# Performance work log

Measured on AMD Instinct MI355X. Metric: run time of the kernel, lower is better.

The kernel has to match this reference:

```python
import jax, jax.numpy as jnp
import numpy as np

B, S, F = 4, 2048, 512
H, DH, OUT = 8, 64, 512  # attention_dim=512 -> head_dim=64
NEG_SLOPE = 0.01


def setup_inputs() -> dict:
    key = jax.random.key(0)
    ks = jax.random.split(key, 9)
    sc_in = 1.0 / np.sqrt(F)
    sc_hd = 1.0 / np.sqrt(H * DH)
    return {
        "x": jax.random.normal(ks[0], (B, S, F), dtype=jnp.float32),
        "Wq": jax.random.normal(ks[1], (F, H, DH), dtype=jnp.float32) * sc_in,
        "bq": jnp.zeros((H, DH), dtype=jnp.float32),
        "Wk": jax.random.normal(ks[2], (F, H, DH), dtype=jnp.float32) * sc_in,
        "bk": jnp.zeros((H, DH), dtype=jnp.float32),
        "Wv": jax.random.normal(ks[3], (F, H, DH), dtype=jnp.float32) * sc_in,
        "bv": jnp.zeros((H, DH), dtype=jnp.float32),
        "Wo": jax.random.normal(ks[4], (H, DH, OUT), dtype=jnp.float32) * sc_hd,
        "bo": jnp.zeros((OUT,), dtype=jnp.float32),
    }


def reference(x, Wq, bq, Wk, bk, Wv, bv, Wo, bo):
    # QKV projections: DenseGeneral(axis=-1, features=(H, DH)) -> [B, S, H, DH]
    q = jnp.einsum('bsf,fhd->bshd', x, Wq) + bq
    k = jnp.einsum('bsf,fhd->bshd', x, Wk) + bk
    v = jnp.einsum('bsf,fhd->bshd', x, Wv) + bv

    # Pairwise squared L2: l2[b,h,i,j] = ||q[b,i,h]-k[b,j,h]||^2
    q2 = jnp.sum(q * q, axis=-1)              # [B, S, H]
    k2 = jnp.sum(k * k, axis=-1)              # [B, S, H]
    qk = jnp.einsum('bihd,bjhd->bhij', q, k)  # [B, H, S, S]
    l2 = (q2.transpose(0, 2, 1)[:, :, :, None]
          + k2.transpose(0, 2, 1)[:, :, None, :]
          - 2.0 * qk)

    # softmax over key axis j, then weights.T @ value (note the transpose:
    # output token index is j, summed over query index i, as in the original)
    w = jax.nn.softmax(-l2, axis=-1)                  # [B, H, Si, Sj]
    attn = jnp.einsum('bhij,bihd->bjhd', w, v)        # [B, S, H, DH]

    # out DenseGeneral contracting (H, DH)
    out = jnp.einsum('bshd,hdo->bso', attn, Wo) + bo
    return jnp.where(out >= 0, out, NEG_SLOPE * out)
```

## Files before the change

### kernel.cpp

```cpp
#include <hip/hip_runtime.h>


typedef __attribute__((ext_vector_type(8))) short bf16x8;
typedef __attribute__((ext_vector_type(4))) float f32x4;
typedef __attribute__((ext_vector_type(4))) unsigned short u16x4;

#define MFMA16 __builtin_amdgcn_mfma_f32_16x16x32_bf16
#define LOG2E 1.4426950408889634f
#define TWO_LOG2E 2.8853900817779268f

__device__ inline unsigned short f2bf(float f) {
  unsigned int u = __float_as_uint(f);
  unsigned int r = 0x7fffu + ((u >> 16) & 1u);
  return (unsigned short)((u + r) >> 16);
}
__device__ inline float bf2f(unsigned short h) {
  return __uint_as_float(((unsigned int)h) << 16);
}
__device__ inline float fexp2(float x) { return __builtin_amdgcn_exp2f(x); }

__device__ inline void gl_lds16(const unsigned short* g, unsigned short* lds) {
  __builtin_amdgcn_global_load_lds(
      (const __attribute__((address_space(1))) unsigned int*)g,
      (__attribute__((address_space(3))) unsigned int*)lds, 16, 0, 0);
}

#define NXB4 (8192*512/4)

__global__ __launch_bounds__(256) void prep(
    const float* __restrict__ x, const float* __restrict__ bq,
    const float* __restrict__ bk, const float* __restrict__ bv,
    unsigned short* __restrict__ xb, float* __restrict__ biasp) {
  int i = blockIdx.x * blockDim.x + threadIdx.x;
  if (i < NXB4) {
    f32x4 v = ((const f32x4*)x)[i];
    u16x4 o;
    o.x = f2bf(v.x); o.y = f2bf(v.y); o.z = f2bf(v.z); o.w = f2bf(v.w);
    ((u16x4*)xb)[i] = o;
    return;
  }
  i -= NXB4;
  if (i < 1536) {
    biasp[i] = (i < 512) ? bq[i] : (i < 1024) ? bk[i - 512] : bv[i - 1024];
  }
}

__global__ __launch_bounds__(256) void packW(
    const float* __restrict__ Wq, const float* __restrict__ Wk,
    const float* __restrict__ Wv, const float* __restrict__ Wo,
    unsigned short* __restrict__ wqkvT, unsigned short* __restrict__ woT) {
  const int m = blockIdx.x >> 6;
  const int n0 = ((blockIdx.x >> 3) & 7) * 64;
  const int f0 = (blockIdx.x & 7) * 64;
  const float* W = (m == 0) ? Wq : (m == 1) ? Wk : (m == 2) ? Wv : Wo;
  __shared__ float tile[64][65];
  const int t = threadIdx.x;
  const int c = t & 63, r4 = t >> 6;
#pragma unroll
  for (int k = 0; k < 16; ++k) {
    const int r = r4 + k * 4;
    tile[r][c] = W[(size_t)(f0 + r) * 512 + n0 + c];
  }
  __syncthreads();
#pragma unroll
  for (int k = 0; k < 16; ++k) {
    const int n_idx = r4 + k * 4, f_idx = c;
    const unsigned short v = f2bf(tile[f_idx][n_idx]);
    if (m < 3)
      wqkvT[(size_t)(m * 512 + n0 + n_idx) * 512 + f0 + f_idx] = v;
    else
      woT[(size_t)(n0 + n_idx) * 512 + f0 + f_idx] = v;
  }
}

template<int MODE>
__global__ __launch_bounds__(256) void gemm_bt(
    const unsigned short* __restrict__ A, const unsigned short* __restrict__ Bt,
    const float* __restrict__ bias,
    unsigned short* __restrict__ o_q, unsigned short* __restrict__ o_k,
    unsigned short* __restrict__ o_v, float* __restrict__ o_f, int K) {
  const int lid = blockIdx.x + blockIdx.y * gridDim.x;
  const int tot = gridDim.x * gridDim.y;
  const int lid2 = (lid & 7) * (tot >> 3) + (lid >> 3);
  const int m0 = (lid2 / gridDim.x) * 128;
  const int n0 = (lid2 % gridDim.x) * 128;
  const int tid = threadIdx.x;
  const int w = tid >> 6, l = tid & 63, lg = l >> 4, ll = l & 15;
  const int wr = w >> 1, wc = w & 1;
  __shared__ unsigned short a_lds[128 * 32];
  __shared__ unsigned short b_lds[128 * 32];
  f32x4 acc[4][4] = {};
  const int nkt = K >> 5;
  for (int kt = 0; kt < nkt; ++kt) {
#pragma unroll
    for (int c = 0; c < 2; ++c) {
      const int cc_base = c * 256 + w * 64;
      const int cc = cc_base + l;
      const int row = cc >> 2, cl = cc & 3;
      gl_lds16(A + (size_t)(m0 + row) * K + kt * 32 + cl * 8, a_lds + cc_base * 8);
      gl_lds16(Bt + (size_t)(n0 + row) * K + kt * 32 + cl * 8, b_lds + cc_base * 8);
    }
    __syncthreads();
    bf16x8 af[4], bfr[4];
#pragma unroll
    for (int mi = 0; mi < 4; ++mi)
      af[mi] = *(const bf16x8*)(a_lds + (wr * 64 + mi * 16 + ll) * 32 + lg * 8);
#pragma unroll
    for (int ni = 0; ni < 4; ++ni)
      bfr[ni] = *(const bf16x8*)(b_lds + (wc * 64 + ni * 16 + ll) * 32 + lg * 8);
#pragma unroll
    for (int mi = 0; mi < 4; ++mi)
#pragma unroll
      for (int ni = 0; ni < 4; ++ni)
        acc[mi][ni] = MFMA16(af[mi], bfr[ni], acc[mi][ni], 0, 0, 0);
    __syncthreads();
  }
#pragma unroll
  for (int mi = 0; mi < 4; ++mi)
#pragma unroll
    for (int ni = 0; ni < 4; ++ni) {
      const int col = n0 + wc * 64 + ni * 16 + ll;
      const float bb = bias[col];
#pragma unroll
      for (int r = 0; r < 4; ++r) {
        const int row = m0 + wr * 64 + mi * 16 + lg * 4 + r;
        float v = acc[mi][ni][r] + bb;
        if (MODE == 0) {
          const int which = col >> 9, h = (col >> 6) & 7, d = col & 63;
          const int b = row >> 11, s = row & 2047;
          if (which == 0) v *= TWO_LOG2E;
          const size_t idx = ((size_t)((b * 8 + h) * 2048 + s)) * 64 + d;
          (which == 0 ? o_q : which == 1 ? o_k : o_v)[idx] = f2bf(v);
        } else {
          v = v >= 0.f ? v : 0.01f * v;
          o_f[(size_t)row * 512 + col] = v;
        }
      }
    }
}

__global__ __launch_bounds__(256) void k2_kernel(const unsigned short* __restrict__ k_g,
                                                 float* __restrict__ k2l_g) {
  const int lane = threadIdx.x & 63;
  const int wid = (blockIdx.x * blockDim.x + threadIdx.x) >> 6;
  const int nw = (gridDim.x * blockDim.x) >> 6;
  for (int row = wid; row < 32 * 2048; row += nw) {
    float v = bf2f(k_g[(size_t)row * 64 + lane]);
    v *= v;
#pragma unroll
    for (int m = 1; m < 64; m <<= 1) v += __shfl_xor(v, m);
    if (lane == 0) k2l_g[row] = LOG2E * v;
  }
}

__global__ __launch_bounds__(256) void transpose_v(const unsigned short* __restrict__ v_g,
                                                   const float* __restrict__ invl_g,
                                                   unsigned short* __restrict__ vt_g) {
  const int bh = blockIdx.x >> 5, st = blockIdx.x & 31;
  const int s0 = st * 64;
  __shared__ unsigned short tile[64][72];
  const int t = threadIdx.x;
  {
    const int sl = t >> 2, cg = t & 3;
    const float sc = invl_g[bh * 2048 + s0 + sl];
    const unsigned short* src = v_g + ((size_t)(bh * 2048 + s0 + sl)) * 64 + cg * 16;
    bf16x8 v0 = *(const bf16x8*)(src);
    bf16x8 v1 = *(const bf16x8*)(src + 8);
#pragma unroll
    for (int e = 0; e < 8; ++e) tile[sl][cg * 16 + e] = f2bf(sc * bf2f((unsigned short)v0[e]));
#pragma unroll
    for (int e = 0; e < 8; ++e) tile[sl][cg * 16 + 8 + e] = f2bf(sc * bf2f((unsigned short)v1[e]));
  }
  __syncthreads();
  {
    const int dl = t >> 2, sg = t & 3;
    bf16x8 o0, o1;
#pragma unroll
    for (int e = 0; e < 8; ++e) o0[e] = (short)tile[sg * 16 + e][dl];
#pragma unroll
    for (int e = 0; e < 8; ++e) o1[e] = (short)tile[sg * 16 + 8 + e][dl];
    unsigned short* dst = vt_g + ((size_t)(bh * 64 + dl)) * 2048 + s0 + sg * 16;
    *(bf16x8*)dst = o0;
    *(bf16x8*)(dst + 8) = o1;
  }
}

__global__ __launch_bounds__(256) void pass1(const unsigned short* __restrict__ q_g,
                                             const unsigned short* __restrict__ k_g,
                                             const float* __restrict__ k2l_g,
                                             float* __restrict__ invl_g) {
  const int bx = blockIdx.x;
  const int bh = (bx & 7) * 4 + ((bx >> 3) >> 4);
  const int ib = (bx >> 3) & 15;
  const int i0 = ib * 128;
  const int tid = threadIdx.x, w = tid >> 6, l = tid & 63, lg = l >> 4, ll = l & 15;
  __shared__ unsigned short k_lds[2][64 * 64];
  __shared__ float k2_lds[2][64];
  const unsigned short* k_bh = k_g + (size_t)bh * 2048 * 64;
  const unsigned short* qrow = q_g + ((size_t)(bh * 2048 + i0 + w * 32 + ll)) * 64;
  const bf16x8 qa00 = *(const bf16x8*)(qrow + lg * 8);
  const bf16x8 qa01 = *(const bf16x8*)(qrow + 32 + lg * 8);
  const bf16x8 qa10 = *(const bf16x8*)(qrow + 1024 + lg * 8);
  const bf16x8 qa11 = *(const bf16x8*)(qrow + 1024 + 32 + lg * 8);
  float lrun0[4] = {0.f, 0.f, 0.f, 0.f};
  float lrun1[4] = {0.f, 0.f, 0.f, 0.f};
  const int cb0 = w * 64, cb1 = 256 + w * 64;
  const int cc0 = cb0 + l, cc1 = cb1 + l;
  const int r0_ = cc0 >> 3, c0_ = cc0 & 7, r1_ = cc1 >> 3, c1_ = cc1 & 7;
  const int so0 = (c0_ ^ (r0_ & 7)) * 8;
  const int so1 = (c1_ ^ (r1_ & 7)) * 8;
  gl_lds16(k_bh + (size_t)r0_ * 64 + so0, &k_lds[0][cb0 * 8]);
  gl_lds16(k_bh + (size_t)r1_ * 64 + so1, &k_lds[0][cb1 * 8]);
  if (tid < 64) k2_lds[0][tid] = k2l_g[bh * 2048 + tid];
  __syncthreads();
  for (int jt = 0; jt < 32; ++jt) {
    const int slot = jt & 1;
    if (jt + 1 < 32) {
      const int j1 = (jt + 1) * 64;
      gl_lds16(k_bh + (size_t)(j1 + r0_) * 64 + so0, &k_lds[slot ^ 1][cb0 * 8]);
      gl_lds16(k_bh + (size_t)(j1 + r1_) * 64 + so1, &k_lds[slot ^ 1][cb1 * 8]);
      if (tid < 64) k2_lds[slot ^ 1][tid] = k2l_g[bh * 2048 + j1 + tid];
    }
#pragma unroll
    for (int nf = 0; nf < 4; ++nf) {
      const int jr = nf * 16 + ll;
      const unsigned short* kb = &k_lds[slot][jr * 64];
      const int sw = jr & 7;
      bf16x8 b0 = *(const bf16x8*)(kb + ((lg ^ sw) * 8));
      bf16x8 b1 = *(const bf16x8*)(kb + (((4 + lg) ^ sw) * 8));
      f32x4 sa0 = {};
      sa0 = MFMA16(qa00, b0, sa0, 0, 0, 0);
      sa0 = MFMA16(qa01, b1, sa0, 0, 0, 0);
      f32x4 sa1 = {};
      sa1 = MFMA16(qa10, b0, sa1, 0, 0, 0);
      sa1 = MFMA16(qa11, b1, sa1, 0, 0, 0);
      const float k2v = k2_lds[slot][jr];
      lrun0[0] += fexp2(sa0[0] - k2v);
      lrun0[1] += fexp2(sa0[1] - k2v);
      lrun0[2] += fexp2(sa0[2] - k2v);
      lrun0[3] += fexp2(sa0[3] - k2v);
      lrun1[0] += fexp2(sa1[0] - k2v);
      lrun1[1] += fexp2(sa1[1] - k2v);
      lrun1[2] += fexp2(sa1[2] - k2v);
      lrun1[3] += fexp2(sa1[3] - k2v);
    }
    __syncthreads();
  }
#pragma unroll
  for (int r = 0; r < 4; ++r) {
    float t0 = lrun0[r], t1 = lrun1[r];
#pragma unroll
    for (int m = 1; m < 16; m <<= 1) { t0 += __shfl_xor(t0, m); t1 += __shfl_xor(t1, m); }
    if (ll == 0) {
      invl_g[bh * 2048 + i0 + w * 32 + lg * 4 + r] = 1.f / t0;
      invl_g[bh * 2048 + i0 + w * 32 + 16 + lg * 4 + r] = 1.f / t1;
    }
  }
}

__global__ __launch_bounds__(256) void pass2(const unsigned short* __restrict__ q_g,
                                             const unsigned short* __restrict__ k_g,
                                             const unsigned short* __restrict__ vt_g,
                                             const float* __restrict__ k2l_g,
                                             unsigned short* __restrict__ part0,
                                             unsigned short* __restrict__ part1,
                                             unsigned short* __restrict__ part2) {
  const int bx = blockIdx.x;
  const int bh = (bx & 7) * 4 + ((bx >> 3) >> 4);
  const int jb = (bx >> 3) & 15;
  const int by = blockIdx.y;
  const int j0 = jb * 128;
  const int it0 = by * 11;
  const int it_end = (by == 2) ? 32 : it0 + 11;
  const int tid = threadIdx.x, w = tid >> 6, l = tid & 63, lg = l >> 4, ll = l & 15;
  __shared__ unsigned short q_lds[2][64 * 64];
  __shared__ unsigned short vt_lds[2][64 * 64];
  __shared__ unsigned short p_lds[128 * 64];
  const unsigned short* q_base = q_g + (size_t)bh * 2048 * 64;
  const unsigned short* vt_base = vt_g + (size_t)bh * 64 * 2048;
  const unsigned short* krow = k_g + ((size_t)(bh * 2048 + j0 + w * 32 + ll)) * 64;
  const bf16x8 ka00 = *(const bf16x8*)(krow + lg * 8);
  const bf16x8 ka01 = *(const bf16x8*)(krow + 32 + lg * 8);
  const bf16x8 ka10 = *(const bf16x8*)(krow + 1024 + lg * 8);
  const bf16x8 ka11 = *(const bf16x8*)(krow + 1024 + 32 + lg * 8);
  float k2v0[4], k2v1[4];
#pragma unroll
  for (int r = 0; r < 4; ++r) {
    k2v0[r] = k2l_g[bh * 2048 + j0 + w * 32 + lg * 4 + r];
    k2v1[r] = k2l_g[bh * 2048 + j0 + w * 32 + 16 + lg * 4 + r];
  }
  f32x4 oacc0[4] = {};
  f32x4 oacc1[4] = {};
  const int pslot = it0 & 1;
#pragma unroll
  for (int c = 0; c < 2; ++c) {
    const int cc_base = c * 256 + w * 64;
    const int cc = cc_base + l;
    const int row = cc >> 3, cl = cc & 7;
    const int csw = (cl ^ (row & 7)) * 8;
    gl_lds16(q_base + (size_t)(it0 * 64 + row) * 64 + csw, &q_lds[pslot][cc_base * 8]);
    gl_lds16(vt_base + (size_t)row * 2048 + it0 * 64 + csw, &vt_lds[pslot][cc_base * 8]);
  }
  __syncthreads();
  for (int it = it0; it < it_end; ++it) {
    const int slot = it & 1;
    if (it + 1 < it_end) {
      const int i1 = (it + 1) * 64;
#pragma unroll
      for (int c = 0; c < 2; ++c) {
        const int cc_base = c * 256 + w * 64;
        const int cc = cc_base + l;
        const int row = cc >> 3, cl = cc & 7;
        const int csw = (cl ^ (row & 7)) * 8;
        gl_lds16(q_base + (size_t)(i1 + row) * 64 + csw, &q_lds[slot ^ 1][cc_base * 8]);
        gl_lds16(vt_base + (size_t)row * 2048 + i1 + csw, &vt_lds[slot ^ 1][cc_base * 8]);
      }
    }
#pragma unroll
    for (int nf = 0; nf < 4; ++nf) {
      const int ir = nf * 16 + ll;
      const unsigned short* qb = &q_lds[slot][ir * 64];
      const int sw = ir & 7;
      bf16x8 b0 = *(const bf16x8*)(qb + ((lg ^ sw) * 8));
      bf16x8 b1 = *(const bf16x8*)(qb + (((4 + lg) ^ sw) * 8));
      f32x4 sa0 = {};
      sa0 = MFMA16(ka00, b0, sa0, 0, 0, 0);
      sa0 = MFMA16(ka01, b1, sa0, 0, 0, 0);
      f32x4 sa1 = {};
      sa1 = MFMA16(ka10, b0, sa1, 0, 0, 0);
      sa1 = MFMA16(ka11, b1, sa1, 0, 0, 0);
#pragma unroll
      for (int r = 0; r < 4; ++r) {
        const float p0 = fexp2(sa0[r] - k2v0[r]);
        const float p1 = fexp2(sa1[r] - k2v1[r]);
        const int ja = w * 32 + lg * 4 + r;
        const int jb2 = ja + 16;
        p_lds[ja * 64 + (ir ^ ((ja & 7) << 3))] =
            (unsigned short)(__float_as_uint(p0) >> 16);
        p_lds[jb2 * 64 + (ir ^ ((jb2 & 7) << 3))] =
            (unsigned short)(__float_as_uint(p1) >> 16);
      }
    }
    {
      const int jr0 = w * 32 + ll;
      const int jr1 = jr0 + 16;
      const int swp = ll & 7;
      const unsigned short* pb0 = p_lds + jr0 * 64;
      const unsigned short* pb1 = p_lds + jr1 * 64;
      bf16x8 pa00 = *(const bf16x8*)(pb0 + ((lg ^ swp) * 8));
      bf16x8 pa01 = *(const bf16x8*)(pb0 + (((4 + lg) ^ swp) * 8));
      bf16x8 pa10 = *(const bf16x8*)(pb1 + ((lg ^ swp) * 8));
      bf16x8 pa11 = *(const bf16x8*)(pb1 + (((4 + lg) ^ swp) * 8));
#pragma unroll
      for (int nf = 0; nf < 4; ++nf) {
        const int dr = nf * 16 + ll;
        const unsigned short* vb = &vt_lds[slot][dr * 64];
        const int sw = dr & 7;
        bf16x8 v0 = *(const bf16x8*)(vb + ((lg ^ sw) * 8));
        bf16x8 v1 = *(const bf16x8*)(vb + (((4 + lg) ^ sw) * 8));
        oacc0[nf] = MFMA16(pa00, v0, oacc0[nf], 0, 0, 0);
        oacc0[nf] = MFMA16(pa01, v1, oacc0[nf], 0, 0, 0);
        oacc1[nf] = MFMA16(pa10, v0, oacc1[nf], 0, 0, 0);
        oacc1[nf] = MFMA16(pa11, v1, oacc1[nf], 0, 0, 0);
      }
    }
    __syncthreads();
  }
  unsigned short* po = (by == 0) ? part0 : (by == 1) ? part1 : part2;
  const int b = bh >> 3, h2 = bh & 7;
#pragma unroll
  for (int nf = 0; nf < 4; ++nf) {
    const int d = nf * 16 + ll;
#pragma unroll
    for (int r = 0; r < 4; ++r) {
      const int j = j0 + w * 32 + lg * 4 + r;
      po[((size_t)(b * 2048 + j)) * 512 + h2 * 64 + d] = f2bf(oacc0[nf][r]);
      po[((size_t)(b * 2048 + j + 16)) * 512 + h2 * 64 + d] = f2bf(oacc1[nf][r]);
    }
  }
}

__global__ __launch_bounds__(256) void combine3(unsigned short* __restrict__ p0,
                                                const unsigned short* __restrict__ p1,
                                                const unsigned short* __restrict__ p2) {
  const int i = blockIdx.x * blockDim.x + threadIdx.x;
  bf16x8 a = ((const bf16x8*)p0)[i];
  bf16x8 b = ((const bf16x8*)p1)[i];
  bf16x8 c = ((const bf16x8*)p2)[i];
  bf16x8 o;
#pragma unroll
  for (int e = 0; e < 8; ++e)
    o[e] = (short)f2bf(bf2f((unsigned short)a[e]) + bf2f((unsigned short)b[e]) +
                       bf2f((unsigned short)c[e]));
  ((bf16x8*)p0)[i] = o;
}

extern "C" void kernel_launch(void* const* d_in, const int* in_sizes, int n_in,
                              void* d_out, int out_size, void* d_ws, size_t ws_size,
                              hipStream_t stream) {
  const float* x  = (const float*)d_in[0];
  const float* Wq = (const float*)d_in[1];
  const float* bq = (const float*)d_in[2];
  const float* Wk = (const float*)d_in[3];
  const float* bk = (const float*)d_in[4];
  const float* Wv = (const float*)d_in[5];
  const float* bv = (const float*)d_in[6];
  const float* Wo = (const float*)d_in[7];
  const float* bo = (const float*)d_in[8];
  float* out = (float*)d_out;
  char* ws = (char*)d_ws;

  unsigned short* xb    = (unsigned short*)(ws);
  unsigned short* wqkvT = (unsigned short*)(ws + 8388608);
  unsigned short* woT   = (unsigned short*)(ws + 9961472);
  float*          biasp = (float*)         (ws + 10485760);
  unsigned short* q_g   = (unsigned short*)(ws + 10493952);
  unsigned short* k_g   = (unsigned short*)(ws + 18882560);
  unsigned short* v_g   = (unsigned short*)(ws + 27271168);
  unsigned short* vt_g  = (unsigned short*)(ws + 35659776);
  float*          k2_g  = (float*)         (ws + 44048384);
  float*          invl_g= (float*)         (ws + 44310528);
  unsigned short* attnb = (unsigned short*)(ws + 44572672);
  if (ws_size < (size_t)52961280) return;

  prep<<<4102, 256, 0, stream>>>(x, bq, bk, bv, xb, biasp);
  packW<<<256, 256, 0, stream>>>(Wq, Wk, Wv, Wo, wqkvT, woT);
  gemm_bt<0><<<dim3(12, 64), 256, 0, stream>>>(xb, wqkvT, biasp, q_g, k_g, v_g, nullptr, 512);
  k2_kernel<<<1024, 256, 0, stream>>>(k_g, k2_g);
  pass1<<<512, 256, 0, stream>>>(q_g, k_g, k2_g, invl_g);
  transpose_v<<<1024, 256, 0, stream>>>(v_g, invl_g, vt_g);
  pass2<<<dim3(512, 3), 256, 0, stream>>>(q_g, k_g, vt_g, k2_g, attnb, xb, v_g);
  combine3<<<2048, 256, 0, stream>>>(attnb, xb, v_g);
  gemm_bt<1><<<dim3(4, 64), 256, 0, stream>>>(attnb, woT, bo, nullptr, nullptr, nullptr, out, 512);
}
```

Before: 157.1 us.

## Double-buffer QKV GEMM LDS tiles and fuse key norm into GEMM epilogue

The bf16 GEMM now uses two LDS buffers. It prefetches the next K-slice with global_load_lds while the MFMAs run on the current slice, instead of load-sync-compute on every step. The separate k2_kernel launch is removed. The per-row squared norm of K is computed in the QKV GEMM epilogue with a 16-lane shuffle reduction and written directly to k2_g. This saves one launch and a full re-read of K, at the cost of doubled LDS use and extra epilogue work in the blocks that compute K columns. The norm is now taken from fp32 values rather than bf16-rounded ones, which slightly changes the numerics.

After: 154.5 us. About the same (-1.6%).

```diff
diff --git a/kernel.cpp b/kernel.cpp
--- a/kernel.cpp
+++ b/kernel.cpp
@@ -78,7 +78,8 @@
     const unsigned short* __restrict__ A, const unsigned short* __restrict__ Bt,
     const float* __restrict__ bias,
     unsigned short* __restrict__ o_q, unsigned short* __restrict__ o_k,
-    unsigned short* __restrict__ o_v, float* __restrict__ o_f, int K) {
+    unsigned short* __restrict__ o_v, float* __restrict__ o_f,
+    float* __restrict__ k2l_g, int K) {
   const int lid = blockIdx.x + blockIdx.y * gridDim.x;
   const int tot = gridDim.x * gridDim.y;
   const int lid2 = (lid & 7) * (tot >> 3) + (lid >> 3);
@@ -87,27 +88,34 @@
   const int tid = threadIdx.x;
   const int w = tid >> 6, l = tid & 63, lg = l >> 4, ll = l & 15;
   const int wr = w >> 1, wc = w & 1;
-  __shared__ unsigned short a_lds[128 * 32];
-  __shared__ unsigned short b_lds[128 * 32];
+  __shared__ unsigned short a_lds[2][128 * 32];
+  __shared__ unsigned short b_lds[2][128 * 32];
   f32x4 acc[4][4] = {};
   const int nkt = K >> 5;
+  const int cb0 = w * 64, cb1 = 256 + w * 64;
+  const int cc0 = cb0 + l, cc1 = cb1 + l;
+  const int ar0 = cc0 >> 2, ac0 = cc0 & 3, ar1 = cc1 >> 2, ac1 = cc1 & 3;
+  gl_lds16(A + (size_t)(m0 + ar0) * K + ac0 * 8, &a_lds[0][cb0 * 8]);
+  gl_lds16(A + (size_t)(m0 + ar1) * K + ac1 * 8, &a_lds[0][cb1 * 8]);
+  gl_lds16(Bt + (size_t)(n0 + ar0) * K + ac0 * 8, &b_lds[0][cb0 * 8]);
+  gl_lds16(Bt + (size_t)(n0 + ar1) * K + ac1 * 8, &b_lds[0][cb1 * 8]);
+  __syncthreads();
   for (int kt = 0; kt < nkt; ++kt) {
-#pragma unroll
-    for (int c = 0; c < 2; ++c) {
-      const int cc_base = c * 256 + w * 64;
-      const int cc = cc_base + l;
-      const int row = cc >> 2, cl = cc & 3;
-      gl_lds16(A + (size_t)(m0 + row) * K + kt * 32 + cl * 8, a_lds + cc_base * 8);
-      gl_lds16(Bt + (size_t)(n0 + row) * K + kt * 32 + cl * 8, b_lds + cc_base * 8);
-    }
-    __syncthreads();
+    const int slot = kt & 1;
+    if (kt + 1 < nkt) {
+      const int k1 = (kt + 1) * 32;
+      gl_lds16(A + (size_t)(m0 + ar0) * K + k1 + ac0 * 8, &a_lds[slot ^ 1][cb0 * 8]);
+      gl_lds16(A + (size_t)(m0 + ar1) * K + k1 + ac1 * 8, &a_lds[slot ^ 1][cb1 * 8]);
+      gl_lds16(Bt + (size_t)(n0 + ar0) * K + k1 + ac0 * 8, &b_lds[slot ^ 1][cb0 * 8]);
+      gl_lds16(Bt + (size_t)(n0 + ar1) * K + k1 + ac1 * 8, &b_lds[slot ^ 1][cb1 * 8]);
+    }
     bf16x8 af[4], bfr[4];
 #pragma unroll
     for (int mi = 0; mi < 4; ++mi)
-      af[mi] = *(const bf16x8*)(a_lds + (wr * 64 + mi * 16 + ll) * 32 + lg * 8);
+      af[mi] = *(const bf16x8*)(&a_lds[slot][(wr * 64 + mi * 16 + ll) * 32 + lg * 8]);
 #pragma unroll
     for (int ni = 0; ni < 4; ++ni)
-      bfr[ni] = *(const bf16x8*)(b_lds + (wc * 64 + ni * 16 + ll) * 32 + lg * 8);
+      bfr[ni] = *(const bf16x8*)(&b_lds[slot][(wc * 64 + ni * 16 + ll) * 32 + lg * 8]);
 #pragma unroll
     for (int mi = 0; mi < 4; ++mi)
 #pragma unroll
@@ -137,19 +145,27 @@
         }
       }
     }
-}
-
-__global__ __launch_bounds__(256) void k2_kernel(const unsigned short* __restrict__ k_g,
-                                                 float* __restrict__ k2l_g) {
-  const int lane = threadIdx.x & 63;
-  const int wid = (blockIdx.x * blockDim.x + threadIdx.x) >> 6;
-  const int nw = (gridDim.x * blockDim.x) >> 6;
-  for (int row = wid; row < 32 * 2048; row += nw) {
-    float v = bf2f(k_g[(size_t)row * 64 + lane]);
-    v *= v;
-#pragma unroll
-    for (int m = 1; m < 64; m <<= 1) v += __shfl_xor(v, m);
-    if (lane == 0) k2l_g[row] = LOG2E * v;
+  if (MODE == 0 && n0 >= 512 && n0 < 1024) {
+    const int h = ((n0 + wc * 64) >> 6) & 7;
+#pragma unroll
+    for (int mi = 0; mi < 4; ++mi)
+#pragma unroll
+      for (int r = 0; r < 4; ++r) {
+        float s2 = 0.f;
+#pragma unroll
+        for (int ni = 0; ni < 4; ++ni) {
+          const int col = n0 + wc * 64 + ni * 16 + ll;
+          const float v = acc[mi][ni][r] + bias[col];
+          s2 += v * v;
+        }
+#pragma unroll
+        for (int m = 1; m < 16; m <<= 1) s2 += __shfl_xor(s2, m);
+        if (ll == 0) {
+          const int row = m0 + wr * 64 + mi * 16 + lg * 4 + r;
+          const int b = row >> 11, s = row & 2047;
+          k2l_g[(size_t)(b * 8 + h) * 2048 + s] = LOG2E * s2;
+        }
+      }
   }
 }
 
@@ -425,11 +441,10 @@
 
   prep<<<4102, 256, 0, stream>>>(x, bq, bk, bv, xb, biasp);
   packW<<<256, 256, 0, stream>>>(Wq, Wk, Wv, Wo, wqkvT, woT);
-  gemm_bt<0><<<dim3(12, 64), 256, 0, stream>>>(xb, wqkvT, biasp, q_g, k_g, v_g, nullptr, 512);
-  k2_kernel<<<1024, 256, 0, stream>>>(k_g, k2_g);
+  gemm_bt<0><<<dim3(12, 64), 256, 0, stream>>>(xb, wqkvT, biasp, q_g, k_g, v_g, nullptr, k2_g, 512);
   pass1<<<512, 256, 0, stream>>>(q_g, k_g, k2_g, invl_g);
   transpose_v<<<1024, 256, 0, stream>>>(v_g, invl_g, vt_g);
   pass2<<<dim3(512, 3), 256, 0, stream>>>(q_g, k_g, vt_g, k2_g, attnb, xb, v_g);
   combine3<<<2048, 256, 0, stream>>>(attnb, xb, v_g);
-  gemm_bt<1><<<dim3(4, 64), 256, 0, stream>>>(attnb, woT, bo, nullptr, nullptr, nullptr, out, 512);
-}
+  gemm_bt<1><<<dim3(4, 64), 256, 0, stream>>>(attnb, woT, bo, nullptr, nullptr, nullptr, out, nullptr, 512);
+}
```
